# Optimization experiments

Measured on AMD Instinct MI355X. Metric: run time of the kernel, lower is better.

## Reference

```python
import jax, jax.numpy as jnp
import numpy as np


def setup_inputs() -> dict:
    key = jax.random.key(0)
    ks = jax.random.split(key, 7)
    B, C, W, H = 4, 256, 128, 128
    s = 1.0 / np.sqrt(C)
    return {
        "x": jax.random.normal(ks[0], (B, C, W, H), dtype=jnp.float32),
        "wq": jax.random.normal(ks[1], (C, C), dtype=jnp.float32) * s,
        "bq": jax.random.normal(ks[2], (C,), dtype=jnp.float32) * s,
        "wk": jax.random.normal(ks[3], (C, C), dtype=jnp.float32) * s,
        "bk": jax.random.normal(ks[4], (C,), dtype=jnp.float32) * s,
        "wv": jax.random.normal(ks[5], (C, C), dtype=jnp.float32) * s,
        "bv": jax.random.normal(ks[6], (C,), dtype=jnp.float32) * s,
    }


def reference(x, wq, bq, wk, bk, wv, bv):
    B, C, W, H = x.shape
    N = W * H
    xf = x.reshape(B, C, N)  # flatten spatial: (B, C, N)
    # 1x1 convs are channel-mixing GEMMs: out[b,o,n] = sum_c w[o,c] x[b,c,n] + b[o]
    q = jnp.einsum('oc,bcn->bon', wq, xf) + bq[:, None]
    k = jnp.einsum('oc,bcn->bon', wk, xf) + bk[:, None]
    v = jnp.einsum('oc,bcn->bon', wv, xf) + bv[:, None]
    # channel-channel energy: (B, C, C)
    energy = jnp.einsum('bcn,bdn->bcd', q, k) / jnp.sqrt(jnp.float32(N))
    attention = jax.nn.softmax(energy, axis=-1)
    out = jnp.einsum('bcd,bdn->bcn', attention, v)
    return out.reshape(B, C, W, H) + x
```

## Files before the change

kernel.cpp:

```cpp
#include <hip/hip_runtime.h>
#include <stdint.h>

#define BB 4
#define CC 256
#define NN 16384
#define NSL 32
#define NT 128

typedef unsigned short u16;
typedef __attribute__((ext_vector_type(8))) __bf16 bf16x8;
typedef __attribute__((ext_vector_type(4))) float f32x4;

__device__ __forceinline__ u16 f2bf(float f) {
  union { float f; uint32_t u; } c;
  c.f = f;
  uint32_t u = c.u;
  return (u16)((u + 0x7fffu + ((u >> 16) & 1u)) >> 16);
}

__device__ __forceinline__ void g2l16(const u16* g, u16* l) {
  __builtin_amdgcn_global_load_lds((__attribute__((address_space(1))) void*)g,
                                   (__attribute__((address_space(3))) void*)l, 16, 0, 0);
}

__device__ __forceinline__ void stage256x32_w8(const u16* src, int stride, u16* lds, int tid) {
  int r = tid >> 2;
  int c = (tid & 3) << 3;
  g2l16(src + (size_t)r * stride + c, lds + r * 32 + c);
  g2l16(src + (size_t)(r + 128) * stride + c, lds + (r + 128) * 32 + c);
}

__device__ __forceinline__ void stage128x32_w8(const u16* src, int stride, u16* lds, int tid) {
  int r = tid >> 2;
  int c = (tid & 3) << 3;
  g2l16(src + (size_t)r * stride + c, lds + r * 32 + c);
}

__device__ __forceinline__ void mfma_tile(const u16* As, const u16* Bs, int mb, int nb,
                                          int l16, int q8, f32x4 acc[4][4]) {
  bf16x8 af[4], bf[4];
#pragma unroll
  for (int i = 0; i < 4; i++) af[i] = *(const bf16x8*)&As[(mb + i * 16 + l16) * 32 + q8];
#pragma unroll
  for (int i = 0; i < 4; i++) bf[i] = *(const bf16x8*)&Bs[(nb + i * 16 + l16) * 32 + q8];
#pragma unroll
  for (int i = 0; i < 4; i++)
#pragma unroll
    for (int j = 0; j < 4; j++)
      acc[i][j] = __builtin_amdgcn_mfma_f32_16x16x32_bf16(af[i], bf[j], acc[i][j], 0, 0, 0);
}

__global__ __launch_bounds__(256) void prep_kernel(const float* __restrict__ x,
                                                   u16* __restrict__ xb,
                                                   u16* __restrict__ xbT,
                                                   float* __restrict__ s_part) {
  __shared__ float t[64][129];
  __shared__ float rs[64][4];
  int n0 = blockIdx.x * 128, c0 = blockIdx.y * 64, bz = blockIdx.z;
  int tid = threadIdx.x;
  int rl = tid >> 5;
  int ql = (tid & 31) * 4;
  const float* xs = x + ((size_t)bz * CC + c0) * NN + n0;
  u16* xbp = xb + ((size_t)bz * CC + c0) * NN + n0;
#pragma unroll
  for (int cc = rl; cc < 64; cc += 8) {
    float4 v = *(const float4*)&xs[(size_t)cc * NN + ql];
    t[cc][ql] = v.x; t[cc][ql + 1] = v.y; t[cc][ql + 2] = v.z; t[cc][ql + 3] = v.w;
    union { u16 h[4]; uint2 u; } pk;
    pk.h[0] = f2bf(v.x); pk.h[1] = f2bf(v.y); pk.h[2] = f2bf(v.z); pk.h[3] = f2bf(v.w);
    *(uint2*)&xbp[(size_t)cc * NN + ql] = pk.u;
  }
  __syncthreads();
  {
    int r = tid >> 2, q = tid & 3;
    float p = 0.f;
#pragma unroll
    for (int i = 0; i < 32; i++) p += t[r][q * 32 + i];
    rs[r][q] = p;
  }
  u16* od = xbT + ((size_t)bz * NN + n0) * CC + c0;
  int rt = tid >> 4, qt = (tid & 15) * 4;
#pragma unroll
  for (int nn = rt; nn < 128; nn += 16) {
    union { u16 h[4]; uint2 u; } pk;
    pk.h[0] = f2bf(t[qt][nn]); pk.h[1] = f2bf(t[qt + 1][nn]);
    pk.h[2] = f2bf(t[qt + 2][nn]); pk.h[3] = f2bf(t[qt + 3][nn]);
    *(uint2*)&od[(size_t)nn * CC + qt] = pk.u;
  }
  __syncthreads();
  if (tid < 64)
    s_part[((size_t)bz * NT + blockIdx.x) * CC + c0 + tid] =
        rs[tid][0] + rs[tid][1] + rs[tid][2] + rs[tid][3];
}

__global__ __launch_bounds__(512) void gram_kernel(const u16* __restrict__ xb,
                                                   float* __restrict__ Gp) {
  __shared__ u16 As[2][256 * 32];
  int tid = threadIdx.x;
  int d0 = blockIdx.x * 128;
  int sl = blockIdx.y, bz = blockIdx.z;
  const u16* A = xb + (size_t)bz * CC * NN + sl * 512;
  f32x4 acc[4][4] = {};
  int wave = tid >> 6, lane = tid & 63;
  int mb = (wave & 3) * 64, nb = d0 + (wave >> 2) * 64;
  int quad = lane >> 4, l16 = lane & 15, q8 = quad * 8;
  stage256x32_w8(A, NN, As[0], tid);
  __syncthreads();
  for (int t = 0; t < 16; t++) {
    if (t < 15) stage256x32_w8(A + (t + 1) * 32, NN, As[(t + 1) & 1], tid);
    mfma_tile(As[t & 1], As[t & 1], mb, nb, l16, q8, acc);
    __syncthreads();
  }
  float* gp = Gp + ((size_t)sl * BB + bz) * CC * CC;
#pragma unroll
  for (int i = 0; i < 4; i++)
#pragma unroll
    for (int j = 0; j < 4; j++)
#pragma unroll
      for (int r = 0; r < 4; r++)
        gp[(size_t)(mb + i * 16 + quad * 4 + r) * CC + nb + j * 16 + l16] =
            acc[i][j][r];
}

__global__ __launch_bounds__(256) void reduce_kernel(const float* __restrict__ Gp,
                                                     const float* __restrict__ s_part,
                                                     const float* __restrict__ Wk,
                                                     float* __restrict__ G,
                                                     float* __restrict__ s,
                                                     float* __restrict__ WkT) {
  __shared__ float tw[32][33];
  int t = threadIdx.x, blk = blockIdx.x;
  size_t base = ((size_t)blk * 256 + t) * 4;
  float ax = 0.f, ay = 0.f, az = 0.f, aw = 0.f;
#pragma unroll 8
  for (int sl = 0; sl < NSL; sl++) {
    float4 v = *(const float4*)&Gp[(size_t)sl * (BB * CC * CC) + base];
    ax += v.x; ay += v.y; az += v.z; aw += v.w;
  }
  float4 o; o.x = ax; o.y = ay; o.z = az; o.w = aw;
  *(float4*)&G[base] = o;
  if (blk < BB) {
    float a = 0.f;
#pragma unroll 8
    for (int nt = 0; nt < NT; nt++) a += s_part[((size_t)blk * NT + nt) * CC + t];
    s[blk * CC + t] = a;
  }
  if (blk < 64) {
    int tr = blk >> 3, tc = blk & 7;
    int r = t >> 5, c = t & 31;
#pragma unroll
    for (int i = 0; i < 4; i++)
      tw[r + i * 8][c] = Wk[(size_t)(tr * 32 + r + i * 8) * CC + tc * 32 + c];
    __syncthreads();
#pragma unroll
    for (int i = 0; i < 4; i++)
      WkT[(size_t)(tc * 32 + r + i * 8) * CC + tr * 32 + c] = tw[c][r + i * 8];
  }
}

__global__ __launch_bounds__(512) void mid_kernel(
    const float* __restrict__ G, const float* __restrict__ s,
    const float* __restrict__ Wq, const float* __restrict__ WkT,
    const float* __restrict__ Wv,
    const float* __restrict__ bq, const float* __restrict__ bk,
    const float* __restrict__ bv,
    u16* __restrict__ Mvb, float* __restrict__ bo) {
  __shared__ float sS[CC];
  __shared__ float wqS[4][CC];
  __shared__ float rS[4][CC];
  __shared__ float attS[4][CC];
  __shared__ float part[4][8][CC];
  __shared__ float redA[4][4], redB[4][4], redC[4][4], redD[4][4];
  int t = threadIdx.x;
  int o0 = blockIdx.x * 4, b = blockIdx.y;
  int wv = t >> 6, ln = t & 63;
  int col = t & 255;
  int row_a = t >> 8, row_b = row_a + 2;
  int c4 = ln << 2;
  int d0 = wv << 5;
  if (t < CC) sS[t] = s[b * CC + t];
  {
    const float* wqsrc = Wq + (size_t)o0 * CC;
    ((float*)wqS)[t] = wqsrc[t];
    ((float*)wqS)[t + 512] = wqsrc[t + 512];
  }
  __syncthreads();
  float pa = wqS[row_a][col] * sS[col];
  float pb = wqS[row_b][col] * sS[col];
#pragma unroll
  for (int d = 32; d > 0; d >>= 1) {
    pa += __shfl_xor(pa, d, 64);
    pb += __shfl_xor(pb, d, 64);
  }
  if (ln == 0) { redA[row_a][wv & 3] = pa; redA[row_b][wv & 3] = pb; }
  __syncthreads();
  float up_a = redA[row_a][0] + redA[row_a][1] + redA[row_a][2] + redA[row_a][3] +
               16384.f * bq[o0 + row_a];
  float up_b = redA[row_b][0] + redA[row_b][1] + redA[row_b][2] + redA[row_b][3] +
               16384.f * bq[o0 + row_b];
  const float* Gb = G + (size_t)b * CC * CC;
  {
    f32x4 va[4] = {};
    const float* gp = Gb + (size_t)d0 * CC + c4;
#pragma unroll 8
    for (int i = 0; i < 32; i++) {
      f32x4 g4 = *(const f32x4*)(gp + (size_t)i * CC);
      float w0 = wqS[0][d0 + i], w1 = wqS[1][d0 + i];
      float w2 = wqS[2][d0 + i], w3 = wqS[3][d0 + i];
      va[0] += g4 * w0; va[1] += g4 * w1; va[2] += g4 * w2; va[3] += g4 * w3;
    }
#pragma unroll
    for (int r = 0; r < 4; r++) *(f32x4*)&part[r][wv][c4] = va[r];
  }
  __syncthreads();
  {
    float r_a = bq[o0 + row_a] * sS[col];
    float r_b = bq[o0 + row_b] * sS[col];
#pragma unroll
    for (int w = 0; w < 8; w++) { r_a += part[row_a][w][col]; r_b += part[row_b][w][col]; }
    rS[row_a][col] = r_a;
    rS[row_b][col] = r_b;
  }
  __syncthreads();
  {
    f32x4 ve[4] = {};
    const float* wkp = WkT + (size_t)d0 * CC + c4;
#pragma unroll 8
    for (int i = 0; i < 32; i++) {
      f32x4 w4 = *(const f32x4*)(wkp + (size_t)i * CC);
      float r0 = rS[0][d0 + i], r1 = rS[1][d0 + i];
      float r2 = rS[2][d0 + i], r3 = rS[3][d0 + i];
      ve[0] += w4 * r0; ve[1] += w4 * r1; ve[2] += w4 * r2; ve[3] += w4 * r3;
    }
#pragma unroll
    for (int r = 0; r < 4; r++) *(f32x4*)&part[r][wv][c4] = ve[r];
  }
  __syncthreads();
  float bkc = bk[col];
  float e_a = up_a * bkc, e_b = up_b * bkc;
#pragma unroll
  for (int w = 0; w < 8; w++) { e_a += part[row_a][w][col]; e_b += part[row_b][w][col]; }
  e_a *= 0.0078125f;
  e_b *= 0.0078125f;
  float m_a = e_a, m_b = e_b;
#pragma unroll
  for (int d = 32; d > 0; d >>= 1) {
    m_a = fmaxf(m_a, __shfl_xor(m_a, d, 64));
    m_b = fmaxf(m_b, __shfl_xor(m_b, d, 64));
  }
  if (ln == 0) { redB[row_a][wv & 3] = m_a; redB[row_b][wv & 3] = m_b; }
  __syncthreads();
  m_a = fmaxf(fmaxf(redB[row_a][0], redB[row_a][1]), fmaxf(redB[row_a][2], redB[row_a][3]));
  m_b = fmaxf(fmaxf(redB[row_b][0], redB[row_b][1]), fmaxf(redB[row_b][2], redB[row_b][3]));
  e_a = __expf(e_a - m_a);
  e_b = __expf(e_b - m_b);
  float s_a = e_a, s_b = e_b;
#pragma unroll
  for (int d = 32; d > 0; d >>= 1) {
    s_a += __shfl_xor(s_a, d, 64);
    s_b += __shfl_xor(s_b, d, 64);
  }
  if (ln == 0) { redC[row_a][wv & 3] = s_a; redC[row_b][wv & 3] = s_b; }
  __syncthreads();
  float inv_a = 1.f / (redC[row_a][0] + redC[row_a][1] + redC[row_a][2] + redC[row_a][3]);
  float inv_b = 1.f / (redC[row_b][0] + redC[row_b][1] + redC[row_b][2] + redC[row_b][3]);
  float at_a = e_a * inv_a, at_b = e_b * inv_b;
  attS[row_a][col] = at_a;
  attS[row_b][col] = at_b;
  float bvc = bv[col];
  float ba = at_a * bvc, bb = at_b * bvc;
#pragma unroll
  for (int d = 32; d > 0; d >>= 1) {
    ba += __shfl_xor(ba, d, 64);
    bb += __shfl_xor(bb, d, 64);
  }
  if (ln == 0) { redD[row_a][wv & 3] = ba; redD[row_b][wv & 3] = bb; }
  __syncthreads();
  if (t < 4) bo[b * CC + o0 + t] = redD[t][0] + redD[t][1] + redD[t][2] + redD[t][3];
  {
    f32x4 vm[4] = {};
    const float* wp = Wv + (size_t)d0 * CC + c4;
#pragma unroll 8
    for (int i = 0; i < 32; i++) {
      f32x4 w4 = *(const f32x4*)(wp + (size_t)i * CC);
      float a0 = attS[0][d0 + i], a1 = attS[1][d0 + i];
      float a2 = attS[2][d0 + i], a3 = attS[3][d0 + i];
      vm[0] += w4 * a0; vm[1] += w4 * a1; vm[2] += w4 * a2; vm[3] += w4 * a3;
    }
#pragma unroll
    for (int r = 0; r < 4; r++) *(f32x4*)&part[r][wv][c4] = vm[r];
  }
  __syncthreads();
  float mv_a = 0.f, mv_b = 0.f;
#pragma unroll
  for (int w = 0; w < 8; w++) { mv_a += part[row_a][w][col]; mv_b += part[row_b][w][col]; }
  Mvb[((size_t)b * CC + o0 + row_a) * CC + col] = f2bf(mv_a);
  Mvb[((size_t)b * CC + o0 + row_b) * CC + col] = f2bf(mv_b);
}

__global__ __launch_bounds__(512, 4) void out_kernel(const u16* __restrict__ Mvb,
                                                     const u16* __restrict__ xbT,
                                                     const float* __restrict__ bo,
                                                     const float* __restrict__ x,
                                                     float* __restrict__ out) {
  __shared__ union {
    struct { u16 As[2][256 * 32]; u16 Bs[2][128 * 32]; } st;
    float scr[8][64][20];
  } sm;
  int tid = threadIdx.x;
  int n0 = blockIdx.x * 128, bz = blockIdx.y;
  const u16* A = Mvb + (size_t)bz * CC * CC;
  const u16* Bt = xbT + ((size_t)bz * NN + n0) * CC;
  f32x4 acc[4][4] = {};
  int wave = tid >> 6, lane = tid & 63;
  int mb = (wave & 3) * 64, nb = (wave >> 2) * 64;
  int quad = lane >> 4, l16 = lane & 15, q8 = quad * 8;
  stage256x32_w8(A, CC, sm.st.As[0], tid);
  stage128x32_w8(Bt, CC, sm.st.Bs[0], tid);
  __syncthreads();
  for (int t = 0; t < 8; t++) {
    if (t < 7) {
      stage256x32_w8(A + (t + 1) * 32, CC, sm.st.As[(t + 1) & 1], tid);
      stage128x32_w8(Bt + (t + 1) * 32, CC, sm.st.Bs[(t + 1) & 1], tid);
    }
    mfma_tile(sm.st.As[t & 1], sm.st.Bs[t & 1], mb, nb, l16, q8, acc);
    __syncthreads();
  }
  int l4 = lane >> 2;
  int cgl = lane & 3;
  float bc[4];
#pragma unroll
  for (int kq = 0; kq < 4; kq++) bc[kq] = bo[bz * CC + mb + kq * 16 + l4];
#pragma unroll
  for (int j = 0; j < 4; j++) {
#pragma unroll
    for (int i = 0; i < 4; i++)
#pragma unroll
      for (int r = 0; r < 4; r++)
        sm.scr[wave][i * 16 + quad * 4 + r][l16] = acc[i][j][r];
#pragma unroll
    for (int kq = 0; kq < 4; kq++) {
      int rloc = kq * 16 + l4;
      f32x4 v4 = *(const f32x4*)&sm.scr[wave][rloc][cgl * 4];
      int cg = mb + rloc;
      int ng = n0 + nb + j * 16 + cgl * 4;
      size_t idx = ((size_t)bz * CC + cg) * NN + ng;
      float4 xv = *(const float4*)&x[idx];
      float4 o4;
      o4.x = v4[0] + bc[kq] + xv.x;
      o4.y = v4[1] + bc[kq] + xv.y;
      o4.z = v4[2] + bc[kq] + xv.z;
      o4.w = v4[3] + bc[kq] + xv.w;
      *(float4*)&out[idx] = o4;
    }
  }
}

extern "C" void kernel_launch(void* const* d_in, const int* in_sizes, int n_in,
                              void* d_out, int out_size, void* d_ws, size_t ws_size,
                              hipStream_t stream) {
  (void)in_sizes; (void)n_in; (void)out_size; (void)ws_size;
  const float* x = (const float*)d_in[0];
  const float* wq = (const float*)d_in[1];
  const float* bq = (const float*)d_in[2];
  const float* wk = (const float*)d_in[3];
  const float* bk = (const float*)d_in[4];
  const float* wv = (const float*)d_in[5];
  const float* bv = (const float*)d_in[6];
  float* out = (float*)d_out;

  char* ws = (char*)d_ws;
  u16* xb      = (u16*)(ws + 0);
  u16* xbT     = (u16*)(ws + 33554432);
  float* Gp    = (float*)(ws + 67108864);
  float* G     = (float*)(ws + 100663296);
  float* s_prt = (float*)(ws + 101711872);
  float* s     = (float*)(ws + 102760448);
  u16* Mvb     = (u16*)(ws + 102764544);
  float* bo    = (float*)(ws + 103288832);
  float* WkT   = (float*)(ws + 103292928);

  prep_kernel<<<dim3(NN / 128, CC / 64, BB), 256, 0, stream>>>(x, xb, xbT, s_prt);
  gram_kernel<<<dim3(2, NSL, BB), 512, 0, stream>>>(xb, Gp);
  reduce_kernel<<<256, 256, 0, stream>>>(Gp, s_prt, wk, G, s, WkT);
  mid_kernel<<<dim3(CC / 4, BB), 512, 0, stream>>>(G, s, wq, WkT, wv, bq, bk, bv, Mvb, bo);
  out_kernel<<<dim3(NN / 128, BB), 512, 0, stream>>>(Mvb, xbT, bo, x, out);
}
```

Before: 205.4 us.

## Triple-buffer LDS staging in gram and out kernels; split out_kernel M tile

Both GEMM kernels switch from double to triple-buffered global-to-LDS staging. Waits use explicit vmcnt counts and raw s_barrier, so two tiles stay in flight while one is computed. out_kernel now uses 256-thread blocks with a 128x128 output tile and an extra grid dimension over channels. This doubles the block count for occupancy but loads each xbT tile twice. The hand-written waitcnt and barrier sequence risks ordering errors.

```diff
diff --git a/kernel.cpp b/kernel.cpp
--- a/kernel.cpp
+++ b/kernel.cpp
@@ -11,6 +11,9 @@
 typedef __attribute__((ext_vector_type(8))) __bf16 bf16x8;
 typedef __attribute__((ext_vector_type(4))) float f32x4;
 
+#define WAITV(N) asm volatile("s_waitcnt vmcnt(" #N ")" ::: "memory")
+#define BARRIER() asm volatile("s_barrier" ::: "memory")
+
 __device__ __forceinline__ u16 f2bf(float f) {
   union { float f; uint32_t u; } c;
   c.f = f;
@@ -30,10 +33,11 @@
   g2l16(src + (size_t)(r + 128) * stride + c, lds + (r + 128) * 32 + c);
 }
 
-__device__ __forceinline__ void stage128x32_w8(const u16* src, int stride, u16* lds, int tid) {
+__device__ __forceinline__ void stage128x32_w4(const u16* src, int stride, u16* lds, int tid) {
   int r = tid >> 2;
   int c = (tid & 3) << 3;
   g2l16(src + (size_t)r * stride + c, lds + r * 32 + c);
+  g2l16(src + (size_t)(r + 64) * stride + c, lds + (r + 64) * 32 + c);
 }
 
 __device__ __forceinline__ void mfma_tile(const u16* As, const u16* Bs, int mb, int nb,
@@ -95,7 +99,7 @@
 
 __global__ __launch_bounds__(512) void gram_kernel(const u16* __restrict__ xb,
                                                    float* __restrict__ Gp) {
-  __shared__ u16 As[2][256 * 32];
+  __shared__ u16 As[3][256 * 32];
   int tid = threadIdx.x;
   int d0 = blockIdx.x * 128;
   int sl = blockIdx.y, bz = blockIdx.z;
@@ -105,11 +109,14 @@
   int mb = (wave & 3) * 64, nb = d0 + (wave >> 2) * 64;
   int quad = lane >> 4, l16 = lane & 15, q8 = quad * 8;
   stage256x32_w8(A, NN, As[0], tid);
-  __syncthreads();
+  stage256x32_w8(A + 32, NN, As[1], tid);
+  WAITV(2);
+  BARRIER();
   for (int t = 0; t < 16; t++) {
-    if (t < 15) stage256x32_w8(A + (t + 1) * 32, NN, As[(t + 1) & 1], tid);
-    mfma_tile(As[t & 1], As[t & 1], mb, nb, l16, q8, acc);
-    __syncthreads();
+    if (t < 14) stage256x32_w8(A + (t + 2) * 32, NN, As[(t + 2) % 3], tid);
+    mfma_tile(As[t % 3], As[t % 3], mb, nb, l16, q8, acc);
+    if (t < 14) { WAITV(2); BARRIER(); }
+    else if (t == 14) { WAITV(0); BARRIER(); }
   }
   float* gp = Gp + ((size_t)sl * BB + bz) * CC * CC;
 #pragma unroll
@@ -298,39 +305,44 @@
   Mvb[((size_t)b * CC + o0 + row_b) * CC + col] = f2bf(mv_b);
 }
 
-__global__ __launch_bounds__(512, 4) void out_kernel(const u16* __restrict__ Mvb,
+__global__ __launch_bounds__(256, 3) void out_kernel(const u16* __restrict__ Mvb,
                                                      const u16* __restrict__ xbT,
                                                      const float* __restrict__ bo,
                                                      const float* __restrict__ x,
                                                      float* __restrict__ out) {
   __shared__ union {
-    struct { u16 As[2][256 * 32]; u16 Bs[2][128 * 32]; } st;
-    float scr[8][64][20];
+    struct { u16 As[3][128 * 32]; u16 Bs[3][128 * 32]; } st;
+    float scr[4][64][20];
   } sm;
   int tid = threadIdx.x;
-  int n0 = blockIdx.x * 128, bz = blockIdx.y;
-  const u16* A = Mvb + (size_t)bz * CC * CC;
+  int n0 = blockIdx.x * 128, m0 = blockIdx.y * 128, bz = blockIdx.z;
+  const u16* A = Mvb + (size_t)bz * CC * CC + (size_t)m0 * CC;
   const u16* Bt = xbT + ((size_t)bz * NN + n0) * CC;
   f32x4 acc[4][4] = {};
   int wave = tid >> 6, lane = tid & 63;
-  int mb = (wave & 3) * 64, nb = (wave >> 2) * 64;
+  int mb = (wave & 1) * 64, nb = (wave >> 1) * 64;
   int quad = lane >> 4, l16 = lane & 15, q8 = quad * 8;
-  stage256x32_w8(A, CC, sm.st.As[0], tid);
-  stage128x32_w8(Bt, CC, sm.st.Bs[0], tid);
-  __syncthreads();
+  stage128x32_w4(A, CC, sm.st.As[0], tid);
+  stage128x32_w4(Bt, CC, sm.st.Bs[0], tid);
+  stage128x32_w4(A + 32, CC, sm.st.As[1], tid);
+  stage128x32_w4(Bt + 32, CC, sm.st.Bs[1], tid);
+  WAITV(4);
+  BARRIER();
   for (int t = 0; t < 8; t++) {
-    if (t < 7) {
-      stage256x32_w8(A + (t + 1) * 32, CC, sm.st.As[(t + 1) & 1], tid);
-      stage128x32_w8(Bt + (t + 1) * 32, CC, sm.st.Bs[(t + 1) & 1], tid);
+    if (t < 6) {
+      stage128x32_w4(A + (t + 2) * 32, CC, sm.st.As[(t + 2) % 3], tid);
+      stage128x32_w4(Bt + (t + 2) * 32, CC, sm.st.Bs[(t + 2) % 3], tid);
     }
-    mfma_tile(sm.st.As[t & 1], sm.st.Bs[t & 1], mb, nb, l16, q8, acc);
-    __syncthreads();
-  }
+    mfma_tile(sm.st.As[t % 3], sm.st.Bs[t % 3], mb, nb, l16, q8, acc);
+    if (t < 6) { WAITV(4); BARRIER(); }
+    else if (t == 6) { WAITV(0); BARRIER(); }
+  }
+  __syncthreads();
   int l4 = lane >> 2;
   int cgl = lane & 3;
   float bc[4];
 #pragma unroll
-  for (int kq = 0; kq < 4; kq++) bc[kq] = bo[bz * CC + mb + kq * 16 + l4];
+  for (int kq = 0; kq < 4; kq++) bc[kq] = bo[bz * CC + m0 + mb + kq * 16 + l4];
 #pragma unroll
   for (int j = 0; j < 4; j++) {
 #pragma unroll
@@ -342,7 +354,7 @@
     for (int kq = 0; kq < 4; kq++) {
       int rloc = kq * 16 + l4;
       f32x4 v4 = *(const f32x4*)&sm.scr[wave][rloc][cgl * 4];
-      int cg = mb + rloc;
+      int cg = m0 + mb + rloc;
       int ng = n0 + nb + j * 16 + cgl * 4;
       size_t idx = ((size_t)bz * CC + cg) * NN + ng;
       float4 xv = *(const float4*)&x[idx];
@@ -384,5 +396,5 @@
   gram_kernel<<<dim3(2, NSL, BB), 512, 0, stream>>>(xb, Gp);
   reduce_kernel<<<256, 256, 0, stream>>>(Gp, s_prt, wk, G, s, WkT);
   mid_kernel<<<dim3(CC / 4, BB), 512, 0, stream>>>(G, s, wq, WkT, wv, bq, bk, bv, Mvb, bo);
-  out_kernel<<<dim3(NN / 128, BB), 512, 0, stream>>>(Mvb, xbT, bo, x, out);
-}
+  out_kernel<<<dim3(NN / 128, CC / 128, BB), 256, 0, stream>>>(Mvb, xbT, bo, x, out);
+}
```

New measurement: 209.5 us. About the same (+2.0%).
